# Kernel optimization log

Measured on AMD Instinct MI355X. Metric: run time of the kernel, lower is better.

## Reference

```python
import jax, jax.numpy as jnp
import numpy as np

H, C = 2, 128           # heads, out_channels per head
HC = H * C              # 256 concat output dim
D_IN = 256              # in_channels
D_T = 128               # time encoder out_channels
D_MSG = 128
E_DIM = D_MSG + D_T     # edge_dim = 256
N = 50000
E = 200000
MEAN_DT, STD_DT = 0.0, 1.0
SQRT_C = np.float32(np.sqrt(C))


def _time_enc(rel_t, W_t, b_t):
    # TGN TimeEncoder: cos(Linear(rel_t.view(-1,1)))  -> [E, D_T]
    return jnp.cos(rel_t[:, None] * W_t[0] + b_t)


def _seg_softmax(alpha, dst, n_dst):
    # numerically stable scatter-softmax over destination-node segments
    amax = jax.ops.segment_max(alpha, dst, num_segments=n_dst)
    amax = jnp.where(jnp.isfinite(amax), amax, 0.0)
    ex = jnp.exp(alpha - amax[dst])
    denom = jax.ops.segment_sum(ex, dst, num_segments=n_dst)
    return ex / (denom[dst] + 1e-16)


def _transformer_conv(x_src, x_dst, ei, edge_attr, Wq, bq, Wk, bk, Wv, bv, We, Ws, bs):
    n_dst = x_dst.shape[0]
    src, dst = ei[0], ei[1]
    q = (x_dst @ Wq + bq).reshape(n_dst, H, C)
    k = ((x_src @ Wk + bk)[src]).reshape(-1, H, C)      # gather per edge
    v = ((x_src @ Wv + bv)[src]).reshape(-1, H, C)
    e = (edge_attr @ We).reshape(-1, H, C)              # lin_edge (no bias)
    alpha = jnp.sum(q[dst] * (k + e), axis=-1) / SQRT_C  # [E, H]
    alpha = _seg_softmax(alpha, dst, n_dst)
    msg = (v + e) * alpha[..., None]                    # [E, H, C]
    out = jax.ops.segment_sum(msg.reshape(-1, HC), dst, num_segments=n_dst)
    return out + x_dst @ Ws + bs                        # root/skip connection


def setup_inputs() -> dict:
    key = jax.random.key(0)
    ks = jax.random.split(key, 32)
    s = 0.05
    inp = {
        'x_user': jax.random.normal(ks[0], (N, D_IN), jnp.float32),
        'x_item': jax.random.normal(ks[1], (N, D_IN), jnp.float32),
        'last_update_user': jax.random.uniform(ks[2], (N,), jnp.float32) * 100.0,
        'last_update_item': jax.random.uniform(ks[3], (N,), jnp.float32) * 100.0,
        'edge_index_a': jax.random.randint(ks[4], (2, E), 0, N, jnp.int32),
        'edge_index_b': jax.random.randint(ks[5], (2, E), 0, N, jnp.int32),
        't_a': jax.random.uniform(ks[6], (E,), jnp.float32) * 100.0 + 100.0,
        't_b': jax.random.uniform(ks[7], (E,), jnp.float32) * 100.0 + 100.0,
        'msg_a': jax.random.normal(ks[8], (E, D_MSG), jnp.float32),
        'msg_b': jax.random.normal(ks[9], (E, D_MSG), jnp.float32),
        'W_t': jax.random.normal(ks[10], (1, D_T), jnp.float32) * s,
        'b_t': jax.random.normal(ks[11], (D_T,), jnp.float32) * s,
    }
    i = 12
    for suf in ('a', 'b'):
        for nm, shape in (('Wq', (D_IN, HC)), ('bq', (HC,)), ('Wk', (D_IN, HC)), ('bk', (HC,)),
                          ('Wv', (D_IN, HC)), ('bv', (HC,)), ('We', (E_DIM, HC)),
                          ('Ws', (D_IN, HC)), ('bs', (HC,))):
            inp[f'{nm}_{suf}'] = jax.random.normal(ks[i], shape, jnp.float32) * s
            i += 1
    return inp


def reference(x_user, x_item, last_update_user, last_update_item,
              edge_index_a, edge_index_b, t_a, t_b, msg_a, msg_b, W_t, b_t,
              Wq_a, bq_a, Wk_a, bk_a, Wv_a, bv_a, We_a, Ws_a, bs_a,
              Wq_b, bq_b, Wk_b, bk_b, Wv_b, bv_b, We_b, Ws_b, bs_b):
    # edge type a: ('user','to','item');  edge type b: ('item','rev_to','user')
    rel_a = (t_a - last_update_user[edge_index_a[0]] - MEAN_DT) / STD_DT
    ea = jnp.concatenate([_time_enc(rel_a, W_t, b_t), msg_a], axis=-1)
    rel_b = (t_b - last_update_item[edge_index_b[0]] - MEAN_DT) / STD_DT
    eb = jnp.concatenate([_time_enc(rel_b, W_t, b_t), msg_b], axis=-1)
    out_item = _transformer_conv(x_user, x_item, edge_index_a, ea,
                                 Wq_a, bq_a, Wk_a, bk_a, Wv_a, bv_a, We_a, Ws_a, bs_a)
    out_user = _transformer_conv(x_item, x_user, edge_index_b, eb,
                                 Wq_b, bq_b, Wk_b, bk_b, Wv_b, bv_b, We_b, Ws_b, bs_b)
    return out_user, out_item
```

## Files before the change

kernel.cpp:

```cpp
#include <hip/hip_runtime.h>
#include <hip/hip_bf16.h>

#define N_NODES 50000
#define E_EDGES 200000
static constexpr float INV_SQRT_C = 0.08838834764831845f;
static constexpr int NB_NODE = ((N_NODES + 63) / 64) * 4;
static constexpr int NB_EDGE = E_EDGES / 64;
static constexpr int NB_PAIR = 2 * NB_EDGE;
static constexpr int NB_FUSED = NB_NODE + NB_EDGE;
static constexpr int NB_PREP = 40;
static constexpr int NB_CONV = 12500;
static constexpr int NB_CNT  = ((E_EDGES + 255) / 256) * 2;

typedef __attribute__((ext_vector_type(4))) float f32x4;
typedef __attribute__((ext_vector_type(8))) short s16x8;
typedef __attribute__((ext_vector_type(4))) short s16x4;

__device__ __forceinline__ float b2f(unsigned short u) {
  union { unsigned u; float f; } x; x.u = ((unsigned)u) << 16; return x.f;
}
__device__ __forceinline__ short f2b(float f) {
  union { float f; unsigned u; } x; x.f = f;
  unsigned r = x.u + 0x7FFFu + ((x.u >> 16) & 1u);
  return (short)(r >> 16);
}

struct WPtrs { const float* w[10]; };

struct NodeSet {
  const unsigned short* X16[4];
  const float* Xf[4];
  const short* Wt[4];
  const float* bias[4];
  unsigned short* o16[4];
  float* of[4];
};
struct EdgeSet {
  const int* ei; const float* tvec; const float* lu; const float* msg;
  const short* WeT; const int* pos; unsigned short* e16g;
};

__device__ __forceinline__ void node_block(char* smem, int tid, int nb,
                                           const NodeSet& N, int use16) {
  short* As = (short*)smem;
  const int l = tid & 63;
  const int w = tid >> 6;
  const int colb = l & 15;
  const int g = l >> 4;
  const int job = nb / 782;
  const int m0 = (nb - job * 782) * 64;
  const bool fullblk = (m0 + 64 <= N_NODES);
  const short* Wt = N.Wt[job];
  const float* bias = N.bias[job];
  unsigned short* o16 = N.o16[job];
  float* of = N.of[job];

  if (use16) {
    const unsigned short* X = N.X16[job];
    if (fullblk) {
#pragma unroll
      for (int i = 0; i < 4; ++i) {
        int flat = tid + i * 512;
        int r = flat >> 5, cg = flat & 31;
        *(s16x8*)&As[r * 264 + cg * 8] = *(const s16x8*)(X + (size_t)(m0 + r) * 256 + cg * 8);
      }
    } else {
#pragma unroll
      for (int i = 0; i < 4; ++i) {
        int flat = tid + i * 512;
        int r = flat >> 5, cg = flat & 31;
        s16x8 v = (s16x8)(short)0;
        if (m0 + r < N_NODES) v = *(const s16x8*)(X + (size_t)(m0 + r) * 256 + cg * 8);
        *(s16x8*)&As[r * 264 + cg * 8] = v;
      }
    }
  } else {
    const float* X = N.Xf[job];
#pragma unroll
    for (int i = 0; i < 8; ++i) {
      int flat = tid + i * 512;
      int r = flat >> 6, c4 = flat & 63;
      float4 xv = make_float4(0.f, 0.f, 0.f, 0.f);
      if (fullblk || m0 + r < N_NODES) xv = *(const float4*)(X + (size_t)(m0 + r) * 256 + c4 * 4);
      s16x4 sv; sv[0] = f2b(xv.x); sv[1] = f2b(xv.y); sv[2] = f2b(xv.z); sv[3] = f2b(xv.w);
      *(s16x4*)&As[r * 264 + c4 * 4] = sv;
    }
  }
  __syncthreads();

  const short* wbase0 = Wt + (((2 * w + 0) * 8) * 16 + colb) * 32 + g * 8;
  const short* wbase1 = Wt + (((2 * w + 1) * 8) * 16 + colb) * 32 + g * 8;

  f32x4 acc[4][2];
#pragma unroll
  for (int m = 0; m < 4; ++m) { acc[m][0] = (f32x4)(0.0f); acc[m][1] = (f32x4)(0.0f); }
#pragma unroll
  for (int ks = 0; ks < 8; ++ks) {
    s16x8 b0 = *(const s16x8*)(wbase0 + ks * 512);
    s16x8 b1 = *(const s16x8*)(wbase1 + ks * 512);
#pragma unroll
    for (int m = 0; m < 4; ++m) {
      s16x8 a = *(const s16x8*)&As[(16 * m + colb) * 264 + ks * 32 + g * 8];
      acc[m][0] = __builtin_amdgcn_mfma_f32_16x16x32_bf16(a, b0, acc[m][0], 0, 0, 0);
      acc[m][1] = __builtin_amdgcn_mfma_f32_16x16x32_bf16(a, b1, acc[m][1], 0, 0, 0);
    }
  }
  __syncthreads();

  if (of) {
    float* buf = (float*)smem;
#pragma unroll 1
    for (int half = 0; half < 2; ++half) {
#pragma unroll
      for (int j = 0; j < 2; ++j) {
        int col = (2 * w + j) * 16 + colb;
        float bv = bias[col];
#pragma unroll
        for (int mm = 0; mm < 2; ++mm) {
          int m = half * 2 + mm;
#pragma unroll
          for (int r = 0; r < 4; ++r)
            buf[(16 * mm + g * 4 + r) * 260 + col] = acc[m][j][r] + bv;
        }
      }
      __syncthreads();
#pragma unroll
      for (int i = 0; i < 4; ++i) {
        int flat = tid + i * 512;
        int row = flat >> 6, ch = flat & 63;
        int grow = m0 + half * 32 + row;
        if (fullblk || grow < N_NODES)
          *(float4*)(of + (size_t)grow * 256 + ch * 4) = *(const float4*)&buf[row * 260 + ch * 4];
      }
      __syncthreads();
    }
  } else {
    short* buf = (short*)smem;
#pragma unroll
    for (int j = 0; j < 2; ++j) {
      int col = (2 * w + j) * 16 + colb;
      float bv = bias[col];
#pragma unroll
      for (int m = 0; m < 4; ++m)
#pragma unroll
        for (int r = 0; r < 4; ++r)
          buf[(16 * m + g * 4 + r) * 264 + col] = f2b(acc[m][j][r] + bv);
    }
    __syncthreads();
#pragma unroll
    for (int i = 0; i < 4; ++i) {
      int flat = tid + i * 512;
      int row = flat >> 5, ch = flat & 31;
      if (fullblk || m0 + row < N_NODES)
        *(s16x8*)(o16 + (size_t)(m0 + row) * 256 + ch * 8) = *(const s16x8*)&buf[row * 264 + ch * 8];
    }
  }
}

__device__ __forceinline__ void edge_block(char* smem, int tid, int eb,
                                           const EdgeSet& E,
                                           const float* Wtim, const float* btim) {
  short* attr = (short*)smem;
  float* rel  = (float*)(smem + 33792);
  int*   poss = (int*)(smem + 34048);
  const int l = tid & 63;
  const int w = tid >> 6;
  const int colb = l & 15;
  const int g = l >> 4;
  const int e0 = eb * 64;

  const float wt = Wtim[tid & 127], bt = btim[tid & 127];

  if (tid < 64) {
    rel[tid] = E.tvec[e0 + tid] - E.lu[E.ei[e0 + tid]];
    poss[tid] = E.pos[e0 + tid];
  }
#pragma unroll
  for (int i = 0; i < 4; ++i) {
    int flat = tid + i * 512;
    int row = flat >> 5, c4 = flat & 31;
    float4 mv = *(const float4*)(E.msg + (size_t)(e0 + row) * 128 + c4 * 4);
    s16x4 sv; sv[0] = f2b(mv.x); sv[1] = f2b(mv.y); sv[2] = f2b(mv.z); sv[3] = f2b(mv.w);
    *(s16x4*)&attr[row * 264 + 128 + c4 * 4] = sv;
  }
  __syncthreads();

  {
    int col = tid & 127;
    int r0 = (tid >> 7) * 16;
#pragma unroll
    for (int i = 0; i < 16; ++i)
      attr[(r0 + i) * 264 + col] = f2b(__cosf(rel[r0 + i] * wt + bt));
  }
  __syncthreads();

  const short* wbase0 = E.WeT + (((2 * w + 0) * 8) * 16 + colb) * 32 + g * 8;
  const short* wbase1 = E.WeT + (((2 * w + 1) * 8) * 16 + colb) * 32 + g * 8;
  f32x4 acc[4][2];
#pragma unroll
  for (int m = 0; m < 4; ++m) { acc[m][0] = (f32x4)(0.0f); acc[m][1] = (f32x4)(0.0f); }
#pragma unroll
  for (int ks = 0; ks < 8; ++ks) {
    s16x8 b0 = *(const s16x8*)(wbase0 + ks * 512);
    s16x8 b1 = *(const s16x8*)(wbase1 + ks * 512);
#pragma unroll
    for (int m = 0; m < 4; ++m) {
      s16x8 a = *(const s16x8*)&attr[(16 * m + colb) * 264 + ks * 32 + g * 8];
      acc[m][0] = __builtin_amdgcn_mfma_f32_16x16x32_bf16(a, b0, acc[m][0], 0, 0, 0);
      acc[m][1] = __builtin_amdgcn_mfma_f32_16x16x32_bf16(a, b1, acc[m][1], 0, 0, 0);
    }
  }
  __syncthreads();
#pragma unroll
  for (int j = 0; j < 2; ++j)
#pragma unroll
    for (int m = 0; m < 4; ++m)
#pragma unroll
      for (int r = 0; r < 4; ++r)
        attr[(16 * m + g * 4 + r) * 264 + (2 * w + j) * 16 + colb] = f2b(acc[m][j][r]);
  __syncthreads();

#pragma unroll
  for (int i = 0; i < 4; ++i) {
    int flat = tid + i * 512;
    int row = flat >> 5, cg = flat & 31;
    size_t slot = (size_t)poss[row];
    *(s16x8*)(E.e16g + slot * 256 + cg * 8) = *(const s16x8*)&attr[row * 264 + cg * 8];
  }
}

__device__ __forceinline__ void process_dst(
    int d, int c0, const int* __restrict__ start, const unsigned short* __restrict__ esrc,
    const unsigned short* __restrict__ Q16, const unsigned short* __restrict__ K16,
    const unsigned short* __restrict__ V16, const unsigned short* __restrict__ e16,
    float* __restrict__ out)
{
  const int s0 = start[d], s1 = start[d + 1];
  if (s1 <= s0) return;

  s16x4 qv = *(const s16x4*)(Q16 + (size_t)d * 256 + c0);
  const float q0 = b2f((unsigned short)qv[0]), q1 = b2f((unsigned short)qv[1]);
  const float q2 = b2f((unsigned short)qv[2]), q3 = b2f((unsigned short)qv[3]);

  float den = 0.f;
  float a0 = 0.f, a1 = 0.f, a2 = 0.f, a3 = 0.f;
  int p = s0;

#define EDGE_LOAD(J, PP)                                                    \
    int s##J = (int)esrc[PP];                                               \
    s16x4 ev##J = *(const s16x4*)(e16 + (size_t)(PP) * 256 + c0);           \
    s16x4 kv##J = *(const s16x4*)(K16 + (size_t)s##J * 256 + c0);           \
    s16x4 vv##J = *(const s16x4*)(V16 + (size_t)s##J * 256 + c0);           \
    float e0##J = b2f((unsigned short)ev##J[0]), e1##J = b2f((unsigned short)ev##J[1]); \
    float e2##J = b2f((unsigned short)ev##J[2]), e3##J = b2f((unsigned short)ev##J[3]); \
    float dt##J = q0 * (b2f((unsigned short)kv##J[0]) + e0##J)              \
                + q1 * (b2f((unsigned short)kv##J[1]) + e1##J)              \
                + q2 * (b2f((unsigned short)kv##J[2]) + e2##J)              \
                + q3 * (b2f((unsigned short)kv##J[3]) + e3##J);

#define EDGE_ACC(J)                                                         \
    den += ex##J;                                                           \
    a0 += ex##J * (b2f((unsigned short)vv##J[0]) + e0##J);                  \
    a1 += ex##J * (b2f((unsigned short)vv##J[1]) + e1##J);                  \
    a2 += ex##J * (b2f((unsigned short)vv##J[2]) + e2##J);                  \
    a3 += ex##J * (b2f((unsigned short)vv##J[3]) + e3##J);

  for (; p + 4 <= s1; p += 4) {
    EDGE_LOAD(A, p)  EDGE_LOAD(B, p + 1)  EDGE_LOAD(C, p + 2)  EDGE_LOAD(D, p + 3)
    dtA += __shfl_xor(dtA, 1);  dtB += __shfl_xor(dtB, 1);
    dtC += __shfl_xor(dtC, 1);  dtD += __shfl_xor(dtD, 1);
    dtA += __shfl_xor(dtA, 2);  dtB += __shfl_xor(dtB, 2);
    dtC += __shfl_xor(dtC, 2);  dtD += __shfl_xor(dtD, 2);
    dtA += __shfl_xor(dtA, 4);  dtB += __shfl_xor(dtB, 4);
    dtC += __shfl_xor(dtC, 4);  dtD += __shfl_xor(dtD, 4);
    dtA += __shfl_xor(dtA, 8);  dtB += __shfl_xor(dtB, 8);
    dtC += __shfl_xor(dtC, 8);  dtD += __shfl_xor(dtD, 8);
    dtA += __shfl_xor(dtA, 16); dtB += __shfl_xor(dtB, 16);
    dtC += __shfl_xor(dtC, 16); dtD += __shfl_xor(dtD, 16);
    float exA = __expf(dtA * INV_SQRT_C), exB = __expf(dtB * INV_SQRT_C);
    float exC = __expf(dtC * INV_SQRT_C), exD = __expf(dtD * INV_SQRT_C);
    EDGE_ACC(A) EDGE_ACC(B) EDGE_ACC(C) EDGE_ACC(D)
  }
  for (; p < s1; ++p) {
    EDGE_LOAD(T, p)
    dtT += __shfl_xor(dtT, 1);
    dtT += __shfl_xor(dtT, 2);
    dtT += __shfl_xor(dtT, 4);
    dtT += __shfl_xor(dtT, 8);
    dtT += __shfl_xor(dtT, 16);
    float exT = __expf(dtT * INV_SQRT_C);
    EDGE_ACC(T)
  }
#undef EDGE_LOAD
#undef EDGE_ACC

  float inv = 1.f / (den + 1e-16f);
  float4* op = (float4*)(out + (size_t)d * 256 + c0);
  float4 o = *op;
  o.x += a0 * inv; o.y += a1 * inv; o.z += a2 * inv; o.w += a3 * inv;
  *op = o;
}

__global__ __launch_bounds__(256) void setup_fused(
    WPtrs p, short* __restrict__ WtT,
    const float* __restrict__ xu, const float* __restrict__ xi,
    unsigned short* __restrict__ x16u, unsigned short* __restrict__ x16i, int nconv,
    const int* __restrict__ eia, const int* __restrict__ eib, int* __restrict__ counts)
{
  __shared__ short T[256 * 66];
  const int bx = blockIdx.x;
  const int tid = threadIdx.x;

  if (bx < NB_PREP) {
    const int wi = bx >> 2, cq = bx & 3;
    const float* w = p.w[wi];
    short* o = WtT + wi * 65536;
#pragma unroll
    for (int i = 0; i < 64; ++i) {
      int flat = tid + i * 256;
      int k = flat >> 6, cc = flat & 63;
      T[k * 66 + cc] = f2b(w[k * 256 + cq * 64 + cc]);
    }
    __syncthreads();
#pragma unroll
    for (int i = 0; i < 8; ++i) {
      int flat2 = tid + i * 256;
      int g = flat2 & 3, colb = (flat2 >> 2) & 15, ks = (flat2 >> 6) & 7, ctl = flat2 >> 9;
      int ct = cq * 4 + ctl;
      s16x8 v;
#pragma unroll
      for (int j = 0; j < 8; ++j)
        v[j] = T[(ks * 32 + g * 8 + j) * 66 + ctl * 16 + colb];
      *(s16x8*)(o + (((ct * 8 + ks) * 16 + colb) * 32 + g * 8)) = v;
    }
    return;
  }
  int cb = bx - NB_PREP;
  if (cb < nconv) {
    int y = cb >= (nconv / 2);
    int xb = y ? cb - nconv / 2 : cb;
    const float* in = y ? xi : xu;
    unsigned short* out = y ? x16i : x16u;
    size_t base = ((size_t)xb * 256 + tid) * 8;
    float4 a = *(const float4*)(in + base);
    float4 b = *(const float4*)(in + base + 4);
    s16x8 v;
    v[0] = f2b(a.x); v[1] = f2b(a.y); v[2] = f2b(a.z); v[3] = f2b(a.w);
    v[4] = f2b(b.x); v[5] = f2b(b.y); v[6] = f2b(b.z); v[7] = f2b(b.w);
    *(s16x8*)(out + base) = v;
    return;
  }
  cb -= nconv;
  int y = cb >= (NB_CNT / 2);
  int tb = y ? cb - NB_CNT / 2 : cb;
  const int* ei = y ? eib : eia;
  int* c = counts + y * N_NODES;
  int t = tb * 256 + tid;
  if (t < E_EDGES) atomicAdd(&c[ei[E_EDGES + t]], 1);
}

__global__ __launch_bounds__(1024) void csr_scan2(int* __restrict__ counts,
                                                  int* __restrict__ start) {
  int* cnt = counts + blockIdx.x * N_NODES;
  int* st  = start + blockIdx.x * (N_NODES + 1);
  __shared__ int wsum[16];
  __shared__ int chunk_tot;
  __shared__ int carry_s;
  const int tid = threadIdx.x, lane = tid & 63, wid = tid >> 6;
  if (tid == 0) carry_s = 0;
  __syncthreads();
  for (int base = 0; base < N_NODES; base += 1024) {
    int gi = base + tid;
    int x = (gi < N_NODES) ? cnt[gi] : 0;
    int v = x;
#pragma unroll
    for (int d = 1; d < 64; d <<= 1) {
      int t = __shfl_up(v, d);
      if (lane >= d) v += t;
    }
    if (lane == 63) wsum[wid] = v;
    __syncthreads();
    if (tid == 0) {
      int run = 0;
#pragma unroll
      for (int i = 0; i < 16; ++i) { int t = wsum[i]; wsum[i] = run; run += t; }
      chunk_tot = run;
    }
    __syncthreads();
    if (gi < N_NODES) {
      int excl = carry_s + wsum[wid] + v - x;
      st[gi] = excl;
      cnt[gi] = excl;
    }
    __syncthreads();
    if (tid == 0) carry_s += chunk_tot;
  }
  if (tid == 0) st[N_NODES] = carry_s;
}

__global__ __launch_bounds__(256) void csr_fill2(const int* __restrict__ eia,
                                                 const int* __restrict__ eib,
                                                 int* __restrict__ counts,
                                                 int* __restrict__ pos,
                                                 unsigned short* __restrict__ esrc) {
  int t = blockIdx.x * 256 + threadIdx.x;
  const int* ei = blockIdx.y ? eib : eia;
  int* cur = counts + blockIdx.y * N_NODES;
  int* ps  = pos + blockIdx.y * E_EDGES;
  unsigned short* es = esrc + (size_t)blockIdx.y * E_EDGES;
  if (t < E_EDGES) {
    int d = ei[E_EDGES + t];
    int p = atomicAdd(&cur[d], 1);
    ps[t] = p;
    es[p] = (unsigned short)ei[t];
  }
}

struct FusedArgs { NodeSet n; EdgeSet e; const float* Wtim; const float* btim; int use16; };

__global__ __launch_bounds__(512) void fused_ne(FusedArgs A) {
  __shared__ __align__(16) char smem[34816];
  const int bx = blockIdx.x;
  int nb = -1, eb = -1;
  if (bx < NB_PAIR) { if (bx & 1) eb = bx >> 1; else nb = bx >> 1; }
  else nb = NB_EDGE + (bx - NB_PAIR);
  if (nb >= 0) node_block(smem, threadIdx.x, nb, A.n, A.use16);
  else         edge_block(smem, threadIdx.x, eb, A.e, A.Wtim, A.btim);
}

struct MegaNE { NodeSet n[2]; EdgeSet e[2]; const float* Wtim; const float* btim; int use16; };

__global__ __launch_bounds__(512) void mega_ne(MegaNE M) {
  __shared__ __align__(16) char smem[34816];
  const int type = blockIdx.x / NB_FUSED;
  const int bx = blockIdx.x - type * NB_FUSED;
  int nb = -1, eb = -1;
  if (bx < NB_PAIR) { if (bx & 1) eb = bx >> 1; else nb = bx >> 1; }
  else nb = NB_EDGE + (bx - NB_PAIR);
  if (nb >= 0) node_block(smem, threadIdx.x, nb, M.n[type], M.use16);
  else         edge_block(smem, threadIdx.x, eb, M.e[type], M.Wtim, M.btim);
}

__global__ __launch_bounds__(256) void aggregate_fused5(
    const int* __restrict__ start, const unsigned short* __restrict__ esrc,
    const unsigned short* __restrict__ Q16, const unsigned short* __restrict__ K16,
    const unsigned short* __restrict__ V16, const unsigned short* __restrict__ e16,
    float* __restrict__ out)
{
  const int wave = blockIdx.x * 4 + (threadIdx.x >> 6);
  const int nwaves = gridDim.x * 4;
  const int c0 = (threadIdx.x & 63) * 4;
  for (int d = wave; d < N_NODES; d += nwaves)
    process_dst(d, c0, start, esrc, Q16, K16, V16, e16, out);
}

struct MegaAgg {
  const int* start[2]; const unsigned short* esrc[2];
  const unsigned short* Q[2]; const unsigned short* K[2];
  const unsigned short* V[2]; const unsigned short* e16[2];
  float* out[2];
};

__global__ __launch_bounds__(256) void mega_agg(MegaAgg G) {
  const int wave = blockIdx.x * 4 + (threadIdx.x >> 6);
  const int nwaves = gridDim.x * 4;
  const int c0 = (threadIdx.x & 63) * 4;
  for (int dg = wave; dg < 2 * N_NODES; dg += nwaves) {
    const int type = dg & 1;
    const int d = dg >> 1;
    process_dst(d, c0, G.start[type], G.esrc[type], G.Q[type], G.K[type],
                G.V[type], G.e16[type], G.out[type]);
  }
}

extern "C" void kernel_launch(void* const* d_in, const int* in_sizes, int n_in,
                              void* d_out, int out_size, void* d_ws, size_t ws_size,
                              hipStream_t stream) {
  const float* x_user  = (const float*)d_in[0];
  const float* x_item  = (const float*)d_in[1];
  const float* lu_user = (const float*)d_in[2];
  const float* lu_item = (const float*)d_in[3];
  const int*   ei_a    = (const int*)d_in[4];
  const int*   ei_b    = (const int*)d_in[5];
  const float* t_a     = (const float*)d_in[6];
  const float* t_b     = (const float*)d_in[7];
  const float* msg_a   = (const float*)d_in[8];
  const float* msg_b   = (const float*)d_in[9];
  const float* W_t     = (const float*)d_in[10];
  const float* b_t     = (const float*)d_in[11];
  const float* Wq_a = (const float*)d_in[12]; const float* bq_a = (const float*)d_in[13];
  const float* Wk_a = (const float*)d_in[14]; const float* bk_a = (const float*)d_in[15];
  const float* Wv_a = (const float*)d_in[16]; const float* bv_a = (const float*)d_in[17];
  const float* We_a = (const float*)d_in[18];
  const float* Ws_a = (const float*)d_in[19]; const float* bs_a = (const float*)d_in[20];
  const float* Wq_b = (const float*)d_in[21]; const float* bq_b = (const float*)d_in[22];
  const float* Wk_b = (const float*)d_in[23]; const float* bk_b = (const float*)d_in[24];
  const float* Wv_b = (const float*)d_in[25]; const float* bv_b = (const float*)d_in[26];
  const float* We_b = (const float*)d_in[27];
  const float* Ws_b = (const float*)d_in[28]; const float* bs_b = (const float*)d_in[29];

  float* out_user = (float*)d_out;
  float* out_item = (float*)d_out + (size_t)N_NODES * 256;

  WPtrs wp;
  wp.w[0] = Wq_a; wp.w[1] = Wk_a; wp.w[2] = Wv_a; wp.w[3] = Ws_a; wp.w[4] = We_a;
  wp.w[5] = Wq_b; wp.w[6] = Wk_b; wp.w[7] = Wv_b; wp.w[8] = Ws_b; wp.w[9] = We_b;

  dim3 blk(256);
  dim3 blk512(512);
  dim3 gEt2((E_EDGES + 255) / 256, 2);
  dim3 gAgg(1024);

  char* ws = (char*)d_ws;
  size_t off = 0;
  short* WtT = (short*)(ws + off); off += (size_t)10 * 65536 * 2;
  unsigned short* Q16a = (unsigned short*)(ws + off); off += (size_t)N_NODES * 256 * 2;
  unsigned short* K16a = (unsigned short*)(ws + off); off += (size_t)N_NODES * 256 * 2;
  unsigned short* V16a = (unsigned short*)(ws + off); off += (size_t)N_NODES * 256 * 2;
  unsigned short* e16a = (unsigned short*)(ws + off); off += (size_t)E_EDGES * 256 * 2;
  int* pos    = (int*)(ws + off); off += (size_t)2 * E_EDGES * 4;
  int* counts = (int*)(ws + off); off += (size_t)2 * N_NODES * 4;
  int* startb = (int*)(ws + off); off += (size_t)2 * (N_NODES + 1) * 4;
  unsigned short* esrc = (unsigned short*)(ws + off); off += (size_t)2 * E_EDGES * 2;
  const size_t off_base = off;
  unsigned short* X16u = (unsigned short*)(ws + off); off += (size_t)N_NODES * 256 * 2;
  unsigned short* X16i = (unsigned short*)(ws + off); off += (size_t)N_NODES * 256 * 2;
  const size_t off_t1 = off;
  unsigned short* Q16b = (unsigned short*)(ws + off); off += (size_t)N_NODES * 256 * 2;
  unsigned short* K16b = (unsigned short*)(ws + off); off += (size_t)N_NODES * 256 * 2;
  unsigned short* V16b = (unsigned short*)(ws + off); off += (size_t)N_NODES * 256 * 2;
  unsigned short* e16b = (unsigned short*)(ws + off); off += (size_t)E_EDGES * 256 * 2;
  const size_t off_t2 = off;
  const bool use_x16 = (ws_size >= off_t1);
  const bool use_t2  = (ws_size >= off_t2);
  if (!use_x16 && ws_size < off_base) return;

  const int nconv = use_x16 ? NB_CONV : 0;

  hipMemsetAsync(counts, 0, (size_t)2 * N_NODES * 4, stream);
  setup_fused<<<dim3(NB_PREP + nconv + NB_CNT), blk, 0, stream>>>(
      wp, WtT, x_user, x_item, X16u, X16i, nconv, ei_a, ei_b, counts);
  csr_scan2<<<2, 1024, 0, stream>>>(counts, startb);
  csr_fill2<<<gEt2, blk, 0, stream>>>(ei_a, ei_b, counts, pos, esrc);

  NodeSet na, nb_;
  na.X16[0] = X16u; na.X16[1] = X16u; na.X16[2] = X16i; na.X16[3] = X16i;
  na.Xf[0] = x_user; na.Xf[1] = x_user; na.Xf[2] = x_item; na.Xf[3] = x_item;
  na.Wt[0] = WtT + 1 * 65536; na.Wt[1] = WtT + 2 * 65536;
  na.Wt[2] = WtT + 0 * 65536; na.Wt[3] = WtT + 3 * 65536;
  na.bias[0] = bk_a; na.bias[1] = bv_a; na.bias[2] = bq_a; na.bias[3] = bs_a;
  na.o16[0] = K16a; na.o16[1] = V16a; na.o16[2] = Q16a; na.o16[3] = nullptr;
  na.of[0] = nullptr; na.of[1] = nullptr; na.of[2] = nullptr; na.of[3] = out_item;

  nb_.X16[0] = X16i; nb_.X16[1] = X16i; nb_.X16[2] = X16u; nb_.X16[3] = X16u;
  nb_.Xf[0] = x_item; nb_.Xf[1] = x_item; nb_.Xf[2] = x_user; nb_.Xf[3] = x_user;
  nb_.Wt[0] = WtT + 6 * 65536; nb_.Wt[1] = WtT + 7 * 65536;
  nb_.Wt[2] = WtT + 5 * 65536; nb_.Wt[3] = WtT + 8 * 65536;
  nb_.bias[0] = bk_b; nb_.bias[1] = bv_b; nb_.bias[2] = bq_b; nb_.bias[3] = bs_b;
  nb_.of[0] = nullptr; nb_.of[1] = nullptr; nb_.of[2] = nullptr; nb_.of[3] = out_user;

  EdgeSet ea, eb_;
  ea.ei = ei_a; ea.tvec = t_a; ea.lu = lu_user; ea.msg = msg_a;
  ea.WeT = WtT + 4 * 65536; ea.pos = pos; ea.e16g = e16a;
  eb_.ei = ei_b; eb_.tvec = t_b; eb_.lu = lu_item; eb_.msg = msg_b;
  eb_.WeT = WtT + 9 * 65536; eb_.pos = pos + E_EDGES;

  if (use_t2) {
    nb_.o16[0] = K16b; nb_.o16[1] = V16b; nb_.o16[2] = Q16b;
    eb_.e16g = e16b;
    MegaNE M;
    M.n[0] = na; M.n[1] = nb_; M.e[0] = ea; M.e[1] = eb_;
    M.Wtim = W_t; M.btim = b_t; M.use16 = 1;
    mega_ne<<<dim3(2 * NB_FUSED), blk512, 0, stream>>>(M);
    MegaAgg G;
    G.start[0] = startb; G.start[1] = startb + (N_NODES + 1);
    G.esrc[0] = esrc;    G.esrc[1] = esrc + E_EDGES;
    G.Q[0] = Q16a; G.Q[1] = Q16b; G.K[0] = K16a; G.K[1] = K16b;
    G.V[0] = V16a; G.V[1] = V16b; G.e16[0] = e16a; G.e16[1] = e16b;
    G.out[0] = out_item; G.out[1] = out_user;
    mega_agg<<<dim3(2048), blk, 0, stream>>>(G);
  } else {
    nb_.o16[0] = K16a; nb_.o16[1] = V16a; nb_.o16[2] = Q16a;
    eb_.e16g = e16a;
    FusedArgs Aa; Aa.n = na; Aa.e = ea; Aa.Wtim = W_t; Aa.btim = b_t; Aa.use16 = use_x16 ? 1 : 0;
    fused_ne<<<dim3(NB_FUSED), blk512, 0, stream>>>(Aa);
    aggregate_fused5<<<gAgg, blk, 0, stream>>>(startb, esrc, Q16a, K16a, V16a, e16a, out_item);
    FusedArgs Ab; Ab.n = nb_; Ab.e = eb_; Ab.Wtim = W_t; Ab.btim = b_t; Ab.use16 = use_x16 ? 1 : 0;
    fused_ne<<<dim3(NB_FUSED), blk512, 0, stream>>>(Ab);
    aggregate_fused5<<<gAgg, blk, 0, stream>>>(startb + (N_NODES + 1), esrc + E_EDGES,
        Q16a, K16a, V16a, e16a, out_user);
  }
}
```

Baseline: 578.7 us.

## Overlap type-b edge projection with type-a aggregation and share QKV buffers

Replaces the two mega kernels (both types' node and edge GEMMs, then both aggregations) with a new schedule. Type-a node and edge work runs first. A mixed kernel then interleaves type-b edge-projection blocks with type-a aggregation blocks, so the compute-heavy edge GEMM overlaps the gather-bound aggregation. After that, type-b node projections and type-b aggregation run. Q/K/V buffers are now shared between the two types, which shrinks the workspace needed for the fast path but adds a kernel launch and serialises the node projections.

New measurement: 619.4 us. 1.07x slower.

```diff
diff --git a/kernel.cpp b/kernel.cpp
--- a/kernel.cpp
+++ b/kernel.cpp
@@ -11,6 +11,8 @@
 static constexpr int NB_PREP = 40;
 static constexpr int NB_CONV = 12500;
 static constexpr int NB_CNT  = ((E_EDGES + 255) / 256) * 2;
+static constexpr int AGG_BLOCKS_MEGA = 1536;
+static constexpr int NB_MEGA_EA = 3 * AGG_BLOCKS_MEGA + (NB_EDGE - 2 * AGG_BLOCKS_MEGA);
 
 typedef __attribute__((ext_vector_type(4))) float f32x4;
 typedef __attribute__((ext_vector_type(8))) short s16x8;
@@ -428,17 +430,39 @@
   else         edge_block(smem, threadIdx.x, eb, A.e, A.Wtim, A.btim);
 }
 
-struct MegaNE { NodeSet n[2]; EdgeSet e[2]; const float* Wtim; const float* btim; int use16; };
-
-__global__ __launch_bounds__(512) void mega_ne(MegaNE M) {
+__global__ __launch_bounds__(512) void node_only(NodeSet N, int use16) {
   __shared__ __align__(16) char smem[34816];
-  const int type = blockIdx.x / NB_FUSED;
-  const int bx = blockIdx.x - type * NB_FUSED;
-  int nb = -1, eb = -1;
-  if (bx < NB_PAIR) { if (bx & 1) eb = bx >> 1; else nb = bx >> 1; }
-  else nb = NB_EDGE + (bx - NB_PAIR);
-  if (nb >= 0) node_block(smem, threadIdx.x, nb, M.n[type], M.use16);
-  else         edge_block(smem, threadIdx.x, eb, M.e[type], M.Wtim, M.btim);
+  node_block(smem, threadIdx.x, blockIdx.x, N, use16);
+}
+
+struct MegaEA {
+  EdgeSet e;
+  const float* Wtim; const float* btim;
+  const int* start; const unsigned short* esrc;
+  const unsigned short* Q; const unsigned short* K;
+  const unsigned short* V; const unsigned short* e16;
+  float* out;
+};
+
+__global__ __launch_bounds__(512) void mega_ea(MegaEA M) {
+  __shared__ __align__(16) char smem[34816];
+  const int bx = blockIdx.x;
+  int eb = -1, ab = -1;
+  if (bx < 3 * AGG_BLOCKS_MEGA) {
+    int gp = bx / 3, r = bx - gp * 3;
+    if (r < 2) eb = gp * 2 + r; else ab = gp;
+  } else {
+    eb = 2 * AGG_BLOCKS_MEGA + (bx - 3 * AGG_BLOCKS_MEGA);
+  }
+  if (eb >= 0) {
+    edge_block(smem, threadIdx.x, eb, M.e, M.Wtim, M.btim);
+  } else {
+    const int wave = ab * 8 + (threadIdx.x >> 6);
+    const int nwaves = AGG_BLOCKS_MEGA * 8;
+    const int c0 = (threadIdx.x & 63) * 4;
+    for (int d = wave; d < N_NODES; d += nwaves)
+      process_dst(d, c0, M.start, M.esrc, M.Q, M.K, M.V, M.e16, M.out);
+  }
 }
 
 __global__ __launch_bounds__(256) void aggregate_fused5(
@@ -452,25 +476,6 @@
   const int c0 = (threadIdx.x & 63) * 4;
   for (int d = wave; d < N_NODES; d += nwaves)
     process_dst(d, c0, start, esrc, Q16, K16, V16, e16, out);
-}
-
-struct MegaAgg {
-  const int* start[2]; const unsigned short* esrc[2];
-  const unsigned short* Q[2]; const unsigned short* K[2];
-  const unsigned short* V[2]; const unsigned short* e16[2];
-  float* out[2];
-};
-
-__global__ __launch_bounds__(256) void mega_agg(MegaAgg G) {
-  const int wave = blockIdx.x * 4 + (threadIdx.x >> 6);
-  const int nwaves = gridDim.x * 4;
-  const int c0 = (threadIdx.x & 63) * 4;
-  for (int dg = wave; dg < 2 * N_NODES; dg += nwaves) {
-    const int type = dg & 1;
-    const int d = dg >> 1;
-    process_dst(d, c0, G.start[type], G.esrc[type], G.Q[type], G.K[type],
-                G.V[type], G.e16[type], G.out[type]);
-  }
 }
 
 extern "C" void kernel_launch(void* const* d_in, const int* in_sizes, int n_in,
@@ -509,14 +514,13 @@
   dim3 blk(256);
   dim3 blk512(512);
   dim3 gEt2((E_EDGES + 255) / 256, 2);
-  dim3 gAgg(1024);
 
   char* ws = (char*)d_ws;
   size_t off = 0;
   short* WtT = (short*)(ws + off); off += (size_t)10 * 65536 * 2;
-  unsigned short* Q16a = (unsigned short*)(ws + off); off += (size_t)N_NODES * 256 * 2;
-  unsigned short* K16a = (unsigned short*)(ws + off); off += (size_t)N_NODES * 256 * 2;
-  unsigned short* V16a = (unsigned short*)(ws + off); off += (size_t)N_NODES * 256 * 2;
+  unsigned short* Q16 = (unsigned short*)(ws + off); off += (size_t)N_NODES * 256 * 2;
+  unsigned short* K16 = (unsigned short*)(ws + off); off += (size_t)N_NODES * 256 * 2;
+  unsigned short* V16 = (unsigned short*)(ws + off); off += (size_t)N_NODES * 256 * 2;
   unsigned short* e16a = (unsigned short*)(ws + off); off += (size_t)E_EDGES * 256 * 2;
   int* pos    = (int*)(ws + off); off += (size_t)2 * E_EDGES * 4;
   int* counts = (int*)(ws + off); off += (size_t)2 * N_NODES * 4;
@@ -526,13 +530,10 @@
   unsigned short* X16u = (unsigned short*)(ws + off); off += (size_t)N_NODES * 256 * 2;
   unsigned short* X16i = (unsigned short*)(ws + off); off += (size_t)N_NODES * 256 * 2;
   const size_t off_t1 = off;
-  unsigned short* Q16b = (unsigned short*)(ws + off); off += (size_t)N_NODES * 256 * 2;
-  unsigned short* K16b = (unsigned short*)(ws + off); off += (size_t)N_NODES * 256 * 2;
-  unsigned short* V16b = (unsigned short*)(ws + off); off += (size_t)N_NODES * 256 * 2;
   unsigned short* e16b = (unsigned short*)(ws + off); off += (size_t)E_EDGES * 256 * 2;
-  const size_t off_t2 = off;
+  const size_t off_t2e = off;
   const bool use_x16 = (ws_size >= off_t1);
-  const bool use_t2  = (ws_size >= off_t2);
+  const bool use_t2e = (ws_size >= off_t2e);
   if (!use_x16 && ws_size < off_base) return;
 
   const int nconv = use_x16 ? NB_CONV : 0;
@@ -549,7 +550,7 @@
   na.Wt[0] = WtT + 1 * 65536; na.Wt[1] = WtT + 2 * 65536;
   na.Wt[2] = WtT + 0 * 65536; na.Wt[3] = WtT + 3 * 65536;
   na.bias[0] = bk_a; na.bias[1] = bv_a; na.bias[2] = bq_a; na.bias[3] = bs_a;
-  na.o16[0] = K16a; na.o16[1] = V16a; na.o16[2] = Q16a; na.o16[3] = nullptr;
+  na.o16[0] = K16; na.o16[1] = V16; na.o16[2] = Q16; na.o16[3] = nullptr;
   na.of[0] = nullptr; na.of[1] = nullptr; na.of[2] = nullptr; na.of[3] = out_item;
 
   nb_.X16[0] = X16i; nb_.X16[1] = X16i; nb_.X16[2] = X16u; nb_.X16[3] = X16u;
@@ -557,6 +558,7 @@
   nb_.Wt[0] = WtT + 6 * 65536; nb_.Wt[1] = WtT + 7 * 65536;
   nb_.Wt[2] = WtT + 5 * 65536; nb_.Wt[3] = WtT + 8 * 65536;
   nb_.bias[0] = bk_b; nb_.bias[1] = bv_b; nb_.bias[2] = bq_b; nb_.bias[3] = bs_b;
+  nb_.o16[0] = K16; nb_.o16[1] = V16; nb_.o16[2] = Q16; nb_.o16[3] = nullptr;
   nb_.of[0] = nullptr; nb_.of[1] = nullptr; nb_.of[2] = nullptr; nb_.of[3] = out_user;
 
   EdgeSet ea, eb_;
@@ -564,30 +566,27 @@
   ea.WeT = WtT + 4 * 65536; ea.pos = pos; ea.e16g = e16a;
   eb_.ei = ei_b; eb_.tvec = t_b; eb_.lu = lu_item; eb_.msg = msg_b;
   eb_.WeT = WtT + 9 * 65536; eb_.pos = pos + E_EDGES;
-
-  if (use_t2) {
-    nb_.o16[0] = K16b; nb_.o16[1] = V16b; nb_.o16[2] = Q16b;
-    eb_.e16g = e16b;
-    MegaNE M;
-    M.n[0] = na; M.n[1] = nb_; M.e[0] = ea; M.e[1] = eb_;
-    M.Wtim = W_t; M.btim = b_t; M.use16 = 1;
-    mega_ne<<<dim3(2 * NB_FUSED), blk512, 0, stream>>>(M);
-    MegaAgg G;
-    G.start[0] = startb; G.start[1] = startb + (N_NODES + 1);
-    G.esrc[0] = esrc;    G.esrc[1] = esrc + E_EDGES;
-    G.Q[0] = Q16a; G.Q[1] = Q16b; G.K[0] = K16a; G.K[1] = K16b;
-    G.V[0] = V16a; G.V[1] = V16b; G.e16[0] = e16a; G.e16[1] = e16b;
-    G.out[0] = out_item; G.out[1] = out_user;
-    mega_agg<<<dim3(2048), blk, 0, stream>>>(G);
+  eb_.e16g = use_t2e ? e16b : e16a;
+
+  const int u16 = use_x16 ? 1 : 0;
+
+  FusedArgs Aa; Aa.n = na; Aa.e = ea; Aa.Wtim = W_t; Aa.btim = b_t; Aa.use16 = u16;
+  fused_ne<<<dim3(NB_FUSED), blk512, 0, stream>>>(Aa);
+
+  if (use_t2e) {
+    MegaEA M;
+    M.e = eb_; M.Wtim = W_t; M.btim = b_t;
+    M.start = startb; M.esrc = esrc;
+    M.Q = Q16; M.K = K16; M.V = V16; M.e16 = e16a; M.out = out_item;
+    mega_ea<<<dim3(NB_MEGA_EA), blk512, 0, stream>>>(M);
+    node_only<<<dim3(NB_NODE), blk512, 0, stream>>>(nb_, u16);
+    aggregate_fused5<<<dim3(2048), blk, 0, stream>>>(startb + (N_NODES + 1), esrc + E_EDGES,
+        Q16, K16, V16, e16b, out_user);
   } else {
-    nb_.o16[0] = K16a; nb_.o16[1] = V16a; nb_.o16[2] = Q16a;
-    eb_.e16g = e16a;
-    FusedArgs Aa; Aa.n = na; Aa.e = ea; Aa.Wtim = W_t; Aa.btim = b_t; Aa.use16 = use_x16 ? 1 : 0;
-    fused_ne<<<dim3(NB_FUSED), blk512, 0, stream>>>(Aa);
-    aggregate_fused5<<<gAgg, blk, 0, stream>>>(startb, esrc, Q16a, K16a, V16a, e16a, out_item);
-    FusedArgs Ab; Ab.n = nb_; Ab.e = eb_; Ab.Wtim = W_t; Ab.btim = b_t; Ab.use16 = use_x16 ? 1 : 0;
+    aggregate_fused5<<<dim3(2048), blk, 0, stream>>>(startb, esrc, Q16, K16, V16, e16a, out_item);
+    FusedArgs Ab; Ab.n = nb_; Ab.e = eb_; Ab.Wtim = W_t; Ab.btim = b_t; Ab.use16 = u16;
     fused_ne<<<dim3(NB_FUSED), blk512, 0, stream>>>(Ab);
-    aggregate_fused5<<<gAgg, blk, 0, stream>>>(startb + (N_NODES + 1), esrc + E_EDGES,
-        Q16a, K16a, V16a, e16a, out_user);
-  }
-}
+    aggregate_fused5<<<dim3(2048), blk, 0, stream>>>(startb + (N_NODES + 1), esrc + E_EDGES,
+        Q16, K16, V16, e16a, out_user);
+  }
+}
```
